# Optimization experiments

Hardware: AMD Instinct MI355X
Metric: run time of the kernel (lower is better)

## Reference

```python
import jax, jax.numpy as jnp
import numpy as np
from jax import lax

B, C, N, NB = 64, 512, 1024, 4
BC = C // NB
KS = [3, 5, 7, 9]
LEVEL = 2  # min(2, pywt.dwt_max_level(1024, 8)) = 2
FL = 8  # db4 filter length
DN = ('NCH', 'OIH', 'NCH')
# pywt db4 decomposition filters
DEC_LO = jnp.array([-0.010597401784997278, 0.032883011666982945, 0.030841381835986965,
                    -0.18703481171888114, -0.02798376941698385, 0.6308807679295904,
                    0.7148465705525415, 0.23037781330885523], jnp.float32)
DEC_HI = jnp.array([-0.23037781330885523, 0.7148465705525415, -0.6308807679295904,
                    -0.02798376941698385, 0.18703481171888114, 0.030841381835986965,
                    -0.032883011666982945, -0.010597401784997278], jnp.float32)


def conv1d(x, w, b, pad):
    y = lax.conv_general_dilated(x, w, (1,), [(pad, pad)], dimension_numbers=DN)
    return y + b[None, :, None]


def bn_relu(x, g, beta, eps=1e-5):
    # BatchNorm1d in train mode: batch statistics over (B, L) per channel
    mu = x.mean(axis=(0, 2), keepdims=True)
    var = ((x - mu) ** 2).mean(axis=(0, 2), keepdims=True)
    xn = (x - mu) * lax.rsqrt(var + eps)
    return jax.nn.relu(xn * g[None, :, None] + beta[None, :, None])


def dwt1d(x):
    # single-level pywt-compatible DWT, symmetric mode. x: [B, C, n]
    b, c, n = x.shape
    out = (n + FL - 1) // 2
    p = 2 * (out - 1) - n + FL
    xp = jnp.pad(x, ((0, 0), (0, 0), (p // 2, p - p // 2)), mode='symmetric')
    k = jnp.stack([DEC_LO[::-1], DEC_HI[::-1]])[:, None, :]  # [2,1,FL]
    y = lax.conv_general_dilated(xp.reshape(b * c, 1, -1), k, (2,), 'VALID',
                                 dimension_numbers=DN)
    y = y.reshape(b, c, 2, out)
    return y[:, :, 0], y[:, :, 1]  # (cA, cD)


def idwt1d(lo, hi):
    # single-level inverse DWT; output length = 2*nc - FL + 2
    b, c, nc = lo.shape
    x = jnp.stack([lo, hi], axis=2).reshape(b * c, 2, nc)
    # rec filters = dec filters reversed, so flipped-for-conv == dec filters
    k = jnp.stack([DEC_LO, DEC_HI])[None, :, :]  # [1,2,FL]
    y = lax.conv_general_dilated(x, k, (1,), [(FL - 1, FL - 1)],
                                 lhs_dilation=(2,), dimension_numbers=DN)
    y = y[:, 0, FL - 2: FL - 2 + 2 * nc - FL + 2]
    return y.reshape(b, c, -1)


def decouple(x):
    # TemporalPatternDecoupling: db4 wavedec(level=2) -> reconstruct low-pass-only
    # (long term) and detail-only (short term). Torch detaches before pywt.
    x = lax.stop_gradient(x)
    n = x.shape[-1]
    a, details = x, []
    for _ in range(LEVEL):
        a, d = dwt1d(a)
        details.append(d)
    la, sa = a, jnp.zeros_like(a)
    for d in reversed(details):
        dl = d.shape[-1]
        la = idwt1d(la[..., :dl], jnp.zeros_like(d))
        sa = idwt1d(sa[..., :dl], d)
    return sa[..., :n], la[..., :n]


def setup_inputs() -> dict:
    key = jax.random.key(0)
    ks = jax.random.split(key, 32)
    s = 0.05
    inp = {
        'x': jax.random.normal(ks[0], (B, C, N), jnp.float32),
        'w_init': jax.random.normal(ks[1], (C, C, 1), jnp.float32) * s,
        'b_init': jnp.zeros((C,), jnp.float32),
        'w_pf': jax.random.normal(ks[2], (BC, 2 * BC, 1), jnp.float32) * s,
        'b_pf': jnp.zeros((BC,), jnp.float32),
        'w_fus': jax.random.normal(ks[3], (C, C, 1), jnp.float32) * s,
        'b_fus': jnp.zeros((C,), jnp.float32),
    }
    for i in range(NB):
        inp[f'w_b{i + 1}'] = jax.random.normal(ks[4 + i], (BC, BC, KS[i]), jnp.float32) * s
        inp[f'b_b{i + 1}'] = jnp.zeros((BC,), jnp.float32)
        inp[f'g_b{i + 1}'] = jnp.ones((BC,), jnp.float32)
        inp[f'be_b{i + 1}'] = jnp.zeros((BC,), jnp.float32)
    return inp


def reference(x, w_init, b_init, w_b1, b_b1, g_b1, be_b1, w_b2, b_b2, g_b2, be_b2,
              w_b3, b_b3, g_b3, be_b3, w_b4, b_b4, g_b4, be_b4, w_pf, b_pf,
              w_fus, b_fus):
    identity = x
    h = conv1d(x, w_init, b_init, 0)
    branch_in = jnp.split(h, NB, axis=1)
    wb = [w_b1, w_b2, w_b3, w_b4]
    bb = [b_b1, b_b2, b_b3, b_b4]
    gb = [g_b1, g_b2, g_b3, g_b4]
    beb = [be_b1, be_b2, be_b3, be_b4]
    shorts, longs = [], []
    for i in range(NB):
        y = bn_relu(conv1d(branch_in[i], wb[i], bb[i], KS[i] // 2), gb[i], beb[i])
        s, l = decouple(y)
        shorts.append(s)
        longs.append(l)
    for b in range(1, NB):
        shorts[b] = shorts[b] + shorts[b - 1]
    for b in range(NB - 2, -1, -1):
        longs[b] = longs[b] + longs[b + 1]
    enhanced = [conv1d(jnp.concatenate([shorts[b], longs[b]], axis=1), w_pf, b_pf, 0)
                for b in range(NB)]
    out = conv1d(jnp.concatenate(enhanced, axis=1), w_fus, b_fus, 0)
    return out + identity
```

## Files before the change

kernel.cpp:

```cpp
#include <hip/hip_runtime.h>

typedef float  f32x4 __attribute__((ext_vector_type(4)));
typedef short  s16x8 __attribute__((ext_vector_type(8)));
typedef short  s16x4 __attribute__((ext_vector_type(4)));
typedef unsigned short u16;

struct PtrQuad { const float* p[4]; };

__constant__ float c_lo[8] = {-0.010597401784997278f, 0.032883011666982945f,
                              0.030841381835986965f, -0.18703481171888114f,
                              -0.02798376941698385f, 0.6308807679295904f,
                              0.7148465705525415f,  0.23037781330885523f};
__constant__ float c_hi[8] = {-0.23037781330885523f, 0.7148465705525415f,
                              -0.6308807679295904f, -0.02798376941698385f,
                              0.18703481171888114f, 0.030841381835986965f,
                              -0.032883011666982945f, -0.010597401784997278f};

__device__ __forceinline__ u16 f2bf(float f) {
    unsigned u = __float_as_uint(f);
    u += 0x7fffu + ((u >> 16) & 1u);
    return (u16)(u >> 16);
}
__device__ __forceinline__ float bf2f(u16 h) {
    return __uint_as_float(((unsigned)h) << 16);
}
__device__ __forceinline__ int lds_chunk(int row, int g) {
    return row * 4 + (g ^ ((row >> 1) & 3));
}
__device__ __forceinline__ void gload16(void* lds, const void* g) {
    __builtin_amdgcn_global_load_lds(
        (__attribute__((address_space(1))) const void*)g,
        (__attribute__((address_space(3))) void*)lds,
        16, 0, 0);
}

__global__ __launch_bounds__(256) void gemm_nt_k(
    const u16* __restrict__ A, long aB, int lda,
    const u16* __restrict__ B, long bB, int ldb,
    int K,
    u16* __restrict__ D, long dB, int dj,
    const float* __restrict__ bias)
{
    __shared__ s16x8 As[512];
    __shared__ s16x8 Bs[512];
    const int j0 = blockIdx.x * 128, i0 = blockIdx.y * 128;
    const long bb = blockIdx.z;
    const u16* Ab = A + bb * aB;
    const u16* Bb = B + bb * bB;
    const int tid = threadIdx.x;
    const int srow = tid >> 2, sg = tid & 3;
    const int ssg = sg ^ ((srow >> 1) & 3);
    const int l = tid & 63, w = tid >> 6;
    const int wi = (w >> 1) * 64, wj = (w & 1) * 64;
    const int lr = l & 15, lg = l >> 4;
    char* lA0 = (char*)As + w * 1024;
    char* lA1 = (char*)As + 4096 + w * 1024;
    char* lB0 = (char*)Bs + w * 1024;
    char* lB1 = (char*)Bs + 4096 + w * 1024;
    f32x4 acc[4][4] = {};
    for (int k0 = 0; k0 < K; k0 += 32) {
        __syncthreads();
        gload16(lA0, Ab + (long)(i0 + srow) * lda + k0 + ssg * 8);
        gload16(lA1, Ab + (long)(i0 + srow + 64) * lda + k0 + ssg * 8);
        gload16(lB0, Bb + (long)(j0 + srow) * ldb + k0 + ssg * 8);
        gload16(lB1, Bb + (long)(j0 + srow + 64) * ldb + k0 + ssg * 8);
        __syncthreads();
        s16x8 af[4], bf[4];
        #pragma unroll
        for (int f = 0; f < 4; ++f) {
            af[f] = As[lds_chunk(wi + f * 16 + lr, lg)];
            bf[f] = Bs[lds_chunk(wj + f * 16 + lr, lg)];
        }
        #pragma unroll
        for (int fi = 0; fi < 4; ++fi)
            #pragma unroll
            for (int fj = 0; fj < 4; ++fj)
                acc[fi][fj] = __builtin_amdgcn_mfma_f32_16x16x32_bf16(af[fi], bf[fj], acc[fi][fj], 0, 0, 0);
    }
    u16* Db = D + bb * dB;
    #pragma unroll
    for (int fi = 0; fi < 4; ++fi) {
        const int i = i0 + wi + fi * 16 + lg * 4;
        float b0 = 0, b1 = 0, b2v = 0, b3 = 0;
        if (bias) { b0 = bias[i]; b1 = bias[i + 1]; b2v = bias[i + 2]; b3 = bias[i + 3]; }
        #pragma unroll
        for (int fj = 0; fj < 4; ++fj) {
            const int j = j0 + wj + fj * 16 + lr;
            f32x4 d = acc[fi][fj];
            s16x4 o;
            o[0] = (short)f2bf(d[0] + b0); o[1] = (short)f2bf(d[1] + b1);
            o[2] = (short)f2bf(d[2] + b2v); o[3] = (short)f2bf(d[3] + b3);
            *(s16x4*)(Db + (long)j * dj + i) = o;
        }
    }
}

__global__ __launch_bounds__(256) void gemm_branch4_k(
    const u16* __restrict__ WpAll,
    const u16* __restrict__ H,
    u16* __restrict__ Y,
    const u16* __restrict__ zbuf)
{
    __shared__ s16x8 As[512];
    __shared__ s16x8 Bs[512];
    const int j0 = blockIdx.x * 128;
    const int br = blockIdx.y;
    const long bb = blockIdx.z;
    const int taps = 3 + 2 * br;
    const int pad = 1 + br;
    const u16* Wp = WpAll + (long)(br * br + 2 * br) * 16384;
    const u16* Hb = H + bb * 524288 + 128 * br;
    const int tid = threadIdx.x;
    const int srow = tid >> 2, sg = tid & 3;
    const int ssg = sg ^ ((srow >> 1) & 3);
    const int l = tid & 63, w = tid >> 6;
    const int wi = (w >> 1) * 64, wj = (w & 1) * 64;
    const int lr = l & 15, lg = l >> 4;
    const int lda = taps * 128;
    const int K = taps * 128;
    char* lA0 = (char*)As + w * 1024;
    char* lA1 = (char*)As + 4096 + w * 1024;
    char* lB0 = (char*)Bs + w * 1024;
    char* lB1 = (char*)Bs + 4096 + w * 1024;
    f32x4 acc[4][4] = {};
    for (int k0 = 0; k0 < K; k0 += 32) {
        const int tap = k0 >> 7, kc = k0 & 127;
        const int shift = tap - pad;
        __syncthreads();
        gload16(lA0, Wp + (long)srow * lda + k0 + ssg * 8);
        gload16(lA1, Wp + (long)(srow + 64) * lda + k0 + ssg * 8);
        {
            int n0r = j0 + srow + shift;
            int n1r = n0r + 64;
            const u16* s0 = (n0r >= 0 && n0r < 1024) ? (Hb + (long)n0r * 512 + kc + ssg * 8) : zbuf;
            const u16* s1 = (n1r >= 0 && n1r < 1024) ? (Hb + (long)n1r * 512 + kc + ssg * 8) : zbuf;
            gload16(lB0, s0);
            gload16(lB1, s1);
        }
        __syncthreads();
        s16x8 af[4], bf[4];
        #pragma unroll
        for (int f = 0; f < 4; ++f) {
            af[f] = As[lds_chunk(wi + f * 16 + lr, lg)];
            bf[f] = Bs[lds_chunk(wj + f * 16 + lr, lg)];
        }
        #pragma unroll
        for (int fi = 0; fi < 4; ++fi)
            #pragma unroll
            for (int fj = 0; fj < 4; ++fj)
                acc[fi][fj] = __builtin_amdgcn_mfma_f32_16x16x32_bf16(af[fi], bf[fj], acc[fi][fj], 0, 0, 0);
    }
    u16* Db = Y + bb * 524288 + 128 * br;
    #pragma unroll
    for (int fi = 0; fi < 4; ++fi) {
        const int i = wi + fi * 16 + lg * 4;
        #pragma unroll
        for (int fj = 0; fj < 4; ++fj) {
            const int j = j0 + wj + fj * 16 + lr;
            f32x4 d = acc[fi][fj];
            s16x4 o;
            o[0] = (short)f2bf(d[0]); o[1] = (short)f2bf(d[1]);
            o[2] = (short)f2bf(d[2]); o[3] = (short)f2bf(d[3]);
            *(s16x4*)(Db + (long)j * 512 + i) = o;
        }
    }
}

__global__ __launch_bounds__(256) void gemm_psl_k(
    const u16* __restrict__ Ybn,
    const u16* __restrict__ Bmat,
    u16* __restrict__ PSL)
{
    __shared__ s16x8 As[512];
    __shared__ s16x8 Bs[512];
    int flat = blockIdx.x + 8 * (blockIdx.y + 8 * blockIdx.z);
    int swz = (flat & 7) * 512 + (flat >> 3);
    const int j0 = (swz & 7) * 128;
    const int i0 = ((swz >> 3) & 7) * 128;
    const long bb = swz >> 6;
    const int tid = threadIdx.x;
    const u16* Ab = Ybn + bb * 524288;
    const int srow = tid >> 2, sg = tid & 3;
    const int ssg = sg ^ ((srow >> 1) & 3);
    const int l = tid & 63, w = tid >> 6;
    const int wi = (w >> 1) * 64, wj = (w & 1) * 64;
    const int lr = l & 15, lg = l >> 4;
    char* lA0 = (char*)As + w * 1024;
    char* lA1 = (char*)As + 4096 + w * 1024;
    char* lB0 = (char*)Bs + w * 1024;
    char* lB1 = (char*)Bs + 4096 + w * 1024;
    f32x4 acc[4][4] = {};
    for (int k0 = 0; k0 < 512; k0 += 32) {
        __syncthreads();
        gload16(lA0, Ab + (long)(i0 + srow) * 512 + k0 + ssg * 8);
        gload16(lA1, Ab + (long)(i0 + srow + 64) * 512 + k0 + ssg * 8);
        gload16(lB0, Bmat + (long)(j0 + srow) * 512 + k0 + ssg * 8);
        gload16(lB1, Bmat + (long)(j0 + srow + 64) * 512 + k0 + ssg * 8);
        __syncthreads();
        s16x8 af[4], bf[4];
        #pragma unroll
        for (int f = 0; f < 4; ++f) {
            af[f] = As[lds_chunk(wi + f * 16 + lr, lg)];
            bf[f] = Bs[lds_chunk(wj + f * 16 + lr, lg)];
        }
        #pragma unroll
        for (int fi = 0; fi < 4; ++fi)
            #pragma unroll
            for (int fj = 0; fj < 4; ++fj)
                acc[fi][fj] = __builtin_amdgcn_mfma_f32_16x16x32_bf16(af[fi], bf[fj], acc[fi][fj], 0, 0, 0);
    }
    u16* Db = PSL + bb * 1048576;
    #pragma unroll
    for (int fi = 0; fi < 4; ++fi) {
        const int i = i0 + wi + fi * 16 + lg * 4;
        #pragma unroll
        for (int fj = 0; fj < 4; ++fj) {
            const int j = j0 + wj + fj * 16 + lr;
            f32x4 d = acc[fi][fj];
            s16x4 o;
            o[0] = (short)f2bf(d[0]); o[1] = (short)f2bf(d[1]);
            o[2] = (short)f2bf(d[2]); o[3] = (short)f2bf(d[3]);
            *(s16x4*)(Db + (long)j * 1024 + i) = o;
        }
    }
}

__global__ __launch_bounds__(256) void gemm_time_k(
    const u16* __restrict__ MS, const u16* __restrict__ ML,
    const u16* __restrict__ PSL,
    const float* __restrict__ b2, const float* __restrict__ X,
    float* __restrict__ OUT)
{
    __shared__ s16x8 As[512];
    __shared__ s16x8 Bs[512];
    int flat = blockIdx.x + 4 * (blockIdx.y + 8 * blockIdx.z);
    int swz = (flat & 7) * 256 + (flat >> 3);
    const int j0 = (swz & 3) * 128;
    const int i0 = ((swz >> 2) & 7) * 128;
    const long bb = swz >> 5;
    const int tid = threadIdx.x;
    const int srow = tid >> 2, sg = tid & 3;
    const int ssg = sg ^ ((srow >> 1) & 3);
    const int l = tid & 63, w = tid >> 6;
    const int wi = (w >> 1) * 64, wj = (w & 1) * 64;
    const int lr = l & 15, lg = l >> 4;
    const int klo = (i0 - 96) > 0 ? (i0 - 96) : 0;
    const int khi = (i0 + 224) < 1024 ? (i0 + 224) : 1024;
    char* lA0 = (char*)As + w * 1024;
    char* lA1 = (char*)As + 4096 + w * 1024;
    char* lB0 = (char*)Bs + w * 1024;
    char* lB1 = (char*)Bs + 4096 + w * 1024;
    f32x4 acc[4][4] = {};
    for (int pass = 0; pass < 2; ++pass) {
        const u16* A = pass ? ML : MS;
        const u16* B = PSL + bb * 1048576 + (long)pass * 524288;
        for (int k0 = klo; k0 < khi; k0 += 32) {
            __syncthreads();
            gload16(lA0, A + (long)(i0 + srow) * 1024 + k0 + ssg * 8);
            gload16(lA1, A + (long)(i0 + srow + 64) * 1024 + k0 + ssg * 8);
            gload16(lB0, B + (long)(j0 + srow) * 1024 + k0 + ssg * 8);
            gload16(lB1, B + (long)(j0 + srow + 64) * 1024 + k0 + ssg * 8);
            __syncthreads();
            s16x8 af[4], bf[4];
            #pragma unroll
            for (int f = 0; f < 4; ++f) {
                af[f] = As[lds_chunk(wi + f * 16 + lr, lg)];
                bf[f] = Bs[lds_chunk(wj + f * 16 + lr, lg)];
            }
            #pragma unroll
            for (int fi = 0; fi < 4; ++fi)
                #pragma unroll
                for (int fj = 0; fj < 4; ++fj)
                    acc[fi][fj] = __builtin_amdgcn_mfma_f32_16x16x32_bf16(af[fi], bf[fj], acc[fi][fj], 0, 0, 0);
        }
    }
    float* Ob = OUT + bb * 524288;
    const float* Xb = X + bb * 524288;
    #pragma unroll
    for (int fi = 0; fi < 4; ++fi) {
        const int i = i0 + wi + fi * 16 + lg * 4;
        #pragma unroll
        for (int fj = 0; fj < 4; ++fj) {
            const int j = j0 + wj + fj * 16 + lr;
            const long a = (long)j * 1024 + i;
            f32x4 d = acc[fi][fj];
            const float bj = b2[j];
            f32x4 xv = *(const f32x4*)(Xb + a);
            f32x4 o;
            o[0] = d[0] + bj + xv[0]; o[1] = d[1] + bj + xv[1];
            o[2] = d[2] + bj + xv[2]; o[3] = d[3] + bj + xv[3];
            *(f32x4*)(Ob + a) = o;
        }
    }
}

__global__ __launch_bounds__(256) void cast_bf_k(const float* __restrict__ s, u16* __restrict__ d, int n)
{
    int i = blockIdx.x * 256 + threadIdx.x;
    if (i < n) d[i] = f2bf(s[i]);
}

__global__ __launch_bounds__(256) void pack_wb2_k(const float* __restrict__ s, u16* __restrict__ d, int taps)
{
    int i = blockIdx.x * 256 + threadIdx.x;
    if (i >= taps * 16384) return;
    int stride = taps * 128;
    int co = i / stride;
    int rem = i - co * stride;
    int tap = rem >> 7, ci = rem & 127;
    d[i] = f2bf(s[(long)(co * 128 + ci) * taps + tap]);
}

__global__ __launch_bounds__(256) void make_Ucum_k(
    const float* __restrict__ wf, const float* __restrict__ wp,
    u16* __restrict__ USc, u16* __restrict__ ULc)
{
    int gid = blockIdx.x * 256 + threadIdx.x;
    int co = gid >> 7, cc = gid & 127;
    float us[4], ul[4];
    #pragma unroll
    for (int b = 0; b < 4; ++b) {
        float s = 0.f, t = 0.f;
        for (int q = 0; q < 128; ++q) {
            float f = wf[(long)co * 512 + b * 128 + q];
            s += f * wp[q * 256 + cc];
            t += f * wp[q * 256 + 128 + cc];
        }
        us[b] = s; ul[b] = t;
    }
    float suf = 0.f;
    for (int b = 3; b >= 0; --b) { suf += us[b]; USc[(long)co * 512 + b * 128 + cc] = f2bf(suf); }
    float pre = 0.f;
    for (int b = 0; b < 4; ++b) { pre += ul[b]; ULc[(long)co * 512 + b * 128 + cc] = f2bf(pre); }
}

__global__ __launch_bounds__(256) void make_bias2_k(
    const float* __restrict__ wf, const float* __restrict__ bpf,
    const float* __restrict__ bfus, float* __restrict__ b2)
{
    int co = blockIdx.x * 256 + threadIdx.x;
    if (co >= 512) return;
    float s = bfus[co];
    for (int j = 0; j < 512; ++j) s += wf[(long)co * 512 + j] * bpf[j & 127];
    b2[co] = s;
}

__global__ __launch_bounds__(256) void eye_k(float* __restrict__ I)
{
    int i = blockIdx.x * 256 + threadIdx.x;
    I[i] = ((i >> 10) == (i & 1023)) ? 1.0f : 0.0f;
}

__global__ __launch_bounds__(256) void zero_k(float* __restrict__ p, int n)
{
    int i = blockIdx.x * 256 + threadIdx.x;
    if (i < n) p[i] = 0.f;
}

__global__ __launch_bounds__(256) void dwt_k(
    const float* __restrict__ x, float* __restrict__ a, float* __restrict__ d,
    int n_in, int n_out)
{
    const int row = blockIdx.y;
    const int m = blockIdx.x * 256 + threadIdx.x;
    if (m >= n_out) return;
    const float* xr = x + (long)row * n_in;
    float sa = 0.f, sd = 0.f;
    #pragma unroll
    for (int j = 0; j < 8; ++j) {
        int t = 2 * m + 1 - j;
        t = (t < 0) ? (-t - 1) : t;
        t = (t >= n_in) ? (2 * n_in - 1 - t) : t;
        const float v = xr[t];
        sa += v * c_lo[j];
        sd += v * c_hi[j];
    }
    a[(long)row * n_out + m] = sa;
    d[(long)row * n_out + m] = sd;
}

__global__ __launch_bounds__(256) void idwt_k(
    const float* __restrict__ lo, const float* __restrict__ hi,
    float* __restrict__ z, int nc, int n_out, long zB, int zN)
{
    const int row = blockIdx.y;
    const int m = blockIdx.x * 256 + threadIdx.x;
    if (m >= n_out) return;
    const float* lor = lo ? lo + (long)row * nc : nullptr;
    const float* hir = hi ? hi + (long)row * nc : nullptr;
    float s = 0.f;
    #pragma unroll
    for (int k = 0; k < 8; ++k) {
        int t = m + k - 1;
        if (t & 1) continue;
        int j = t >> 1;
        if (j >= nc) continue;
        if (lor) s += c_lo[k] * lor[j];
        if (hir) s += c_hi[k] * hir[j];
    }
    z[(long)(row >> 7) * zB + (long)(row & 127) * zN + m] = s;
}

__global__ __launch_bounds__(256) void trM_k(
    const float* __restrict__ S, const float* __restrict__ L,
    u16* __restrict__ MS, u16* __restrict__ ML)
{
    __shared__ float sh[32][33];
    const float* src = blockIdx.z ? L : S;
    u16* dst = blockIdx.z ? ML : MS;
    const int n0 = blockIdx.x * 32, m0 = blockIdx.y * 32;
    const int tx = threadIdx.x, ty = threadIdx.y;
    #pragma unroll
    for (int k = 0; k < 4; ++k)
        sh[ty + 8 * k][tx] = src[(long)(m0 + ty + 8 * k) * 1024 + n0 + tx];
    __syncthreads();
    #pragma unroll
    for (int k = 0; k < 4; ++k)
        dst[(long)(n0 + ty + 8 * k) * 1024 + m0 + tx] = f2bf(sh[tx][ty + 8 * k]);
}

__global__ __launch_bounds__(256) void trX_k(const float* __restrict__ x, u16* __restrict__ xcl)
{
    __shared__ float sh[32][33];
    const int n0 = blockIdx.x * 32, c0 = blockIdx.y * 32;
    const long bb = blockIdx.z;
    const int tx = threadIdx.x, ty = threadIdx.y;
    const float* xb = x + bb * 524288;
    u16* ob = xcl + bb * 524288;
    #pragma unroll
    for (int k = 0; k < 4; ++k)
        sh[ty + 8 * k][tx] = xb[(long)(c0 + ty + 8 * k) * 1024 + n0 + tx];
    __syncthreads();
    #pragma unroll
    for (int k = 0; k < 4; ++k)
        ob[(long)(n0 + ty + 8 * k) * 512 + c0 + tx] = f2bf(sh[tx][ty + 8 * k]);
}

__global__ __launch_bounds__(256) void bn_stats_k(const u16* __restrict__ Y, float* __restrict__ st)
{
    __shared__ float ss[128][16];
    __shared__ float sq[128][16];
    const int br = blockIdx.y;
    const u16* Yb = Y + 128 * br;
    float* stb = st + br * 256;
    const int t = threadIdx.x;
    const int chg = t & 15, rl = t >> 4;
    const long r0 = (long)blockIdx.x * 256;
    float s[8] = {}, q[8] = {};
    for (int k = 0; k < 16; ++k) {
        long r = r0 + rl + k * 16;
        s16x8 v = *(const s16x8*)(Yb + r * 512 + chg * 8);
        #pragma unroll
        for (int e = 0; e < 8; ++e) { float f = bf2f((u16)v[e]); s[e] += f; q[e] += f * f; }
    }
    #pragma unroll
    for (int e = 0; e < 8; ++e) { ss[chg * 8 + e][rl] = s[e]; sq[chg * 8 + e][rl] = q[e]; }
    __syncthreads();
    if (t < 128) {
        float a = 0, b = 0;
        #pragma unroll
        for (int k = 0; k < 16; ++k) { a += ss[t][k]; b += sq[t][k]; }
        atomicAdd(stb + t, a); atomicAdd(stb + 128 + t, b);
    }
}

__global__ __launch_bounds__(256) void bn_coef_k(
    const float* __restrict__ st, PtrQuad g, PtrQuad be, float* __restrict__ scsh)
{
    int c = blockIdx.x * 256 + threadIdx.x;
    if (c >= 512) return;
    int br = c >> 7, cc = c & 127;
    float mu = st[br * 256 + cc] * (1.0f / 65536.0f);
    float var = st[br * 256 + 128 + cc] * (1.0f / 65536.0f) - mu * mu;
    float sc = g.p[br][cc] * rsqrtf(var + 1e-5f);
    scsh[c] = sc;
    scsh[512 + c] = be.p[br][cc] - mu * sc;
}

__global__ __launch_bounds__(256) void bn_apply_k(
    u16* __restrict__ Y, const float* __restrict__ scsh)
{
    __shared__ float sc_[512];
    __shared__ float sh_[512];
    const int t = threadIdx.x;
    #pragma unroll
    for (int q = 0; q < 2; ++q) {
        sc_[t + q * 256] = scsh[t + q * 256];
        sh_[t + q * 256] = scsh[512 + t + q * 256];
    }
    __syncthreads();
    long gid = (long)blockIdx.x * 256 + t;
    long r = gid >> 6; int cg = (int)(gid & 63);
    u16* p = Y + r * 512 + cg * 8;
    s16x8 v = *(const s16x8*)p;
    #pragma unroll
    for (int e = 0; e < 8; ++e) {
        int c = cg * 8 + e;
        float f = bf2f((u16)v[e]) * sc_[c] + sh_[c];
        v[e] = (short)f2bf(f > 0.f ? f : 0.f);
    }
    *(s16x8*)p = v;
}

extern "C" void kernel_launch(void* const* d_in, const int* in_sizes, int n_in,
                              void* d_out, int out_size, void* d_ws, size_t ws_size,
                              hipStream_t stream)
{
    const float* x      = (const float*)d_in[0];
    const float* w_init = (const float*)d_in[1];
    const float* b_init = (const float*)d_in[2];
    const float* w_pf   = (const float*)d_in[3];
    const float* b_pf   = (const float*)d_in[4];
    const float* w_fus  = (const float*)d_in[5];
    const float* b_fus  = (const float*)d_in[6];
    const float *w_b[4];
    PtrQuad g, be;
    for (int i = 0; i < 4; ++i) {
        w_b[i]  = (const float*)d_in[7 + 4 * i];
        g.p[i]  = (const float*)d_in[9 + 4 * i];
        be.p[i] = (const float*)d_in[10 + 4 * i];
    }
    float* outf = (float*)d_out;

    char* p = (char*)d_ws;
    u16* xcl   = (u16*)p;  p += 67108864;
    u16* h     = (u16*)p;  p += 67108864;
    u16* Y     = (u16*)p;  p += 67108864;
    u16* PSL   = (u16*)p;  p += 134217728;
    u16* Wi    = (u16*)p;  p += 524288;
    u16* Wp    = (u16*)p;  p += 786432;
    u16* UScULc= (u16*)p;  p += 1048576;
    u16* MrowS = (u16*)p;  p += 2097152;
    u16* MrowL = (u16*)p;  p += 2097152;
    float* eye = (float*)p; p += 4194304;
    float* Sid = (float*)p; p += 4194304;
    float* Lid = (float*)p; p += 4194304;
    float* a1  = (float*)p; p += 2109440;
    float* d1  = (float*)p; p += 2109440;
    float* a2  = (float*)p; p += 1069056;
    float* d2  = (float*)p; p += 1069056;
    float* la1 = (float*)p; p += 2109440;
    float* sa1 = (float*)p; p += 2109440;
    float* b2  = (float*)p; p += 2048;
    float* st  = (float*)p; p += 4096;
    float* zbuf= (float*)p; p += 256;
    float* scsh= (float*)p; p += 4096;

    const int KS_[4] = {3, 5, 7, 9};
    const long wpOff[4] = {0, 3 * 16384L, 8 * 16384L, 15 * 16384L};

    cast_bf_k<<<1024, 256, 0, stream>>>(w_init, Wi, 262144);
    for (int br = 0; br < 4; ++br)
        pack_wb2_k<<<(KS_[br] * 16384 + 255) / 256, 256, 0, stream>>>(w_b[br], Wp + wpOff[br], KS_[br]);
    make_Ucum_k<<<256, 256, 0, stream>>>(w_fus, w_pf, UScULc, UScULc + 262144);
    make_bias2_k<<<2, 256, 0, stream>>>(w_fus, b_pf, b_fus, b2);

    eye_k<<<4096, 256, 0, stream>>>(eye);
    dwt_k<<<dim3(3, 1024), 256, 0, stream>>>(eye, a1, d1, 1024, 515);
    dwt_k<<<dim3(2, 1024), 256, 0, stream>>>(a1, a2, d2, 515, 261);
    idwt_k<<<dim3(3, 1024), 256, 0, stream>>>(a2, nullptr, la1, 261, 515, 65920, 515);
    idwt_k<<<dim3(3, 1024), 256, 0, stream>>>(nullptr, d2, sa1, 261, 515, 65920, 515);
    idwt_k<<<dim3(4, 1024), 256, 0, stream>>>(la1, nullptr, Lid, 515, 1024, 131072, 1024);
    idwt_k<<<dim3(4, 1024), 256, 0, stream>>>(sa1, d1, Sid, 515, 1024, 131072, 1024);
    trM_k<<<dim3(32, 32, 2), dim3(32, 8), 0, stream>>>(Sid, Lid, MrowS, MrowL);

    trX_k<<<dim3(32, 16, 64), dim3(32, 8), 0, stream>>>(x, xcl);

    gemm_nt_k<<<dim3(8, 4, 64), 256, 0, stream>>>(Wi, 0, 512, xcl, 524288, 512, 512,
                                                  h, 524288, 512, b_init);

    zero_k<<<5, 256, 0, stream>>>(st, 1088);
    gemm_branch4_k<<<dim3(8, 4, 64), 256, 0, stream>>>(Wp, h, Y, (const u16*)zbuf);

    bn_stats_k<<<dim3(256, 4), 256, 0, stream>>>(Y, st);
    bn_coef_k<<<2, 256, 0, stream>>>(st, g, be, scsh);
    bn_apply_k<<<16384, 256, 0, stream>>>(Y, scsh);

    gemm_psl_k<<<dim3(8, 8, 64), 256, 0, stream>>>(Y, UScULc, PSL);

    gemm_time_k<<<dim3(4, 8, 64), 256, 0, stream>>>(MrowS, MrowL, PSL, b2, x, outf);
}
```

Baseline: 571.5 us.

## Double-buffer LDS in all GEMMs and fuse BN statistics into branch GEMM

Every bf16 MFMA GEMM kernel now uses two LDS buffers. The next K-tile is issued with global_load_lds while the current tile is being multiplied, so each iteration needs one barrier instead of two. The branch convolution GEMM also computes per-channel sum and sum-of-squares from its fp32 accumulators using wave shuffles and writes per-block partials. That removes the separate bn_stats pass over Y and its atomics, and bn_coef now reduces the 512 partials serially per channel. The banded time-domain GEMM also narrows its K window around each row tile, which assumes the level-2 wavelet operator's nonzero band fits within the tighter range.

```diff
diff --git a/kernel.cpp b/kernel.cpp
--- a/kernel.cpp
+++ b/kernel.cpp
@@ -41,8 +41,8 @@
     u16* __restrict__ D, long dB, int dj,
     const float* __restrict__ bias)
 {
-    __shared__ s16x8 As[512];
-    __shared__ s16x8 Bs[512];
+    __shared__ s16x8 As[2][512];
+    __shared__ s16x8 Bs[2][512];
     const int j0 = blockIdx.x * 128, i0 = blockIdx.y * 128;
     const long bb = blockIdx.z;
     const u16* Ab = A + bb * aB;
@@ -53,29 +53,44 @@
     const int l = tid & 63, w = tid >> 6;
     const int wi = (w >> 1) * 64, wj = (w & 1) * 64;
     const int lr = l & 15, lg = l >> 4;
-    char* lA0 = (char*)As + w * 1024;
-    char* lA1 = (char*)As + 4096 + w * 1024;
-    char* lB0 = (char*)Bs + w * 1024;
-    char* lB1 = (char*)Bs + 4096 + w * 1024;
+    const long aoff0 = (long)(i0 + srow) * lda + ssg * 8;
+    const long aoff1 = (long)(i0 + srow + 64) * lda + ssg * 8;
+    const long boff0 = (long)(j0 + srow) * ldb + ssg * 8;
+    const long boff1 = (long)(j0 + srow + 64) * ldb + ssg * 8;
+    const int nt = K >> 5;
     f32x4 acc[4][4] = {};
-    for (int k0 = 0; k0 < K; k0 += 32) {
-        __syncthreads();
-        gload16(lA0, Ab + (long)(i0 + srow) * lda + k0 + ssg * 8);
-        gload16(lA1, Ab + (long)(i0 + srow + 64) * lda + k0 + ssg * 8);
-        gload16(lB0, Bb + (long)(j0 + srow) * ldb + k0 + ssg * 8);
-        gload16(lB1, Bb + (long)(j0 + srow + 64) * ldb + k0 + ssg * 8);
-        __syncthreads();
+    {
+        char* a0 = (char*)&As[0][0] + w * 1024;
+        char* b0 = (char*)&Bs[0][0] + w * 1024;
+        gload16(a0, Ab + aoff0);
+        gload16(a0 + 4096, Ab + aoff1);
+        gload16(b0, Bb + boff0);
+        gload16(b0 + 4096, Bb + boff1);
+    }
+    __syncthreads();
+    for (int t = 0; t < nt; ++t) {
+        const int cur = t & 1;
+        if (t + 1 < nt) {
+            const int k0 = (t + 1) << 5;
+            char* a0 = (char*)&As[cur ^ 1][0] + w * 1024;
+            char* b0 = (char*)&Bs[cur ^ 1][0] + w * 1024;
+            gload16(a0, Ab + aoff0 + k0);
+            gload16(a0 + 4096, Ab + aoff1 + k0);
+            gload16(b0, Bb + boff0 + k0);
+            gload16(b0 + 4096, Bb + boff1 + k0);
+        }
         s16x8 af[4], bf[4];
         #pragma unroll
         for (int f = 0; f < 4; ++f) {
-            af[f] = As[lds_chunk(wi + f * 16 + lr, lg)];
-            bf[f] = Bs[lds_chunk(wj + f * 16 + lr, lg)];
+            af[f] = As[cur][lds_chunk(wi + f * 16 + lr, lg)];
+            bf[f] = Bs[cur][lds_chunk(wj + f * 16 + lr, lg)];
         }
         #pragma unroll
         for (int fi = 0; fi < 4; ++fi)
             #pragma unroll
             for (int fj = 0; fj < 4; ++fj)
                 acc[fi][fj] = __builtin_amdgcn_mfma_f32_16x16x32_bf16(af[fi], bf[fj], acc[fi][fj], 0, 0, 0);
+        __syncthreads();
     }
     u16* Db = D + bb * dB;
     #pragma unroll
@@ -99,10 +114,13 @@
     const u16* __restrict__ WpAll,
     const u16* __restrict__ H,
     u16* __restrict__ Y,
-    const u16* __restrict__ zbuf)
-{
-    __shared__ s16x8 As[512];
-    __shared__ s16x8 Bs[512];
+    const u16* __restrict__ zbuf,
+    float* __restrict__ part)
+{
+    __shared__ s16x8 As[2][512];
+    __shared__ s16x8 Bs[2][512];
+    __shared__ float sred[2][128];
+    __shared__ float qred[2][128];
     const int j0 = blockIdx.x * 128;
     const int br = blockIdx.y;
     const long bb = blockIdx.z;
@@ -117,38 +135,40 @@
     const int wi = (w >> 1) * 64, wj = (w & 1) * 64;
     const int lr = l & 15, lg = l >> 4;
     const int lda = taps * 128;
-    const int K = taps * 128;
-    char* lA0 = (char*)As + w * 1024;
-    char* lA1 = (char*)As + 4096 + w * 1024;
-    char* lB0 = (char*)Bs + w * 1024;
-    char* lB1 = (char*)Bs + 4096 + w * 1024;
-    f32x4 acc[4][4] = {};
-    for (int k0 = 0; k0 < K; k0 += 32) {
+    const int nt = taps * 4;
+    auto stage = [&](int buf, int t) {
+        const int k0 = t << 5;
         const int tap = k0 >> 7, kc = k0 & 127;
         const int shift = tap - pad;
-        __syncthreads();
-        gload16(lA0, Wp + (long)srow * lda + k0 + ssg * 8);
-        gload16(lA1, Wp + (long)(srow + 64) * lda + k0 + ssg * 8);
-        {
-            int n0r = j0 + srow + shift;
-            int n1r = n0r + 64;
-            const u16* s0 = (n0r >= 0 && n0r < 1024) ? (Hb + (long)n0r * 512 + kc + ssg * 8) : zbuf;
-            const u16* s1 = (n1r >= 0 && n1r < 1024) ? (Hb + (long)n1r * 512 + kc + ssg * 8) : zbuf;
-            gload16(lB0, s0);
-            gload16(lB1, s1);
-        }
-        __syncthreads();
+        char* a0 = (char*)&As[buf][0] + w * 1024;
+        char* b0 = (char*)&Bs[buf][0] + w * 1024;
+        gload16(a0, Wp + (long)srow * lda + k0 + ssg * 8);
+        gload16(a0 + 4096, Wp + (long)(srow + 64) * lda + k0 + ssg * 8);
+        int n0r = j0 + srow + shift;
+        int n1r = n0r + 64;
+        const u16* s0 = (n0r >= 0 && n0r < 1024) ? (Hb + (long)n0r * 512 + kc + ssg * 8) : zbuf;
+        const u16* s1 = (n1r >= 0 && n1r < 1024) ? (Hb + (long)n1r * 512 + kc + ssg * 8) : zbuf;
+        gload16(b0, s0);
+        gload16(b0 + 4096, s1);
+    };
+    f32x4 acc[4][4] = {};
+    stage(0, 0);
+    __syncthreads();
+    for (int t = 0; t < nt; ++t) {
+        const int cur = t & 1;
+        if (t + 1 < nt) stage(cur ^ 1, t + 1);
         s16x8 af[4], bf[4];
         #pragma unroll
         for (int f = 0; f < 4; ++f) {
-            af[f] = As[lds_chunk(wi + f * 16 + lr, lg)];
-            bf[f] = Bs[lds_chunk(wj + f * 16 + lr, lg)];
+            af[f] = As[cur][lds_chunk(wi + f * 16 + lr, lg)];
+            bf[f] = Bs[cur][lds_chunk(wj + f * 16 + lr, lg)];
         }
         #pragma unroll
         for (int fi = 0; fi < 4; ++fi)
             #pragma unroll
             for (int fj = 0; fj < 4; ++fj)
                 acc[fi][fj] = __builtin_amdgcn_mfma_f32_16x16x32_bf16(af[fi], bf[fj], acc[fi][fj], 0, 0, 0);
+        __syncthreads();
     }
     u16* Db = Y + bb * 524288 + 128 * br;
     #pragma unroll
@@ -164,6 +184,38 @@
             *(s16x4*)(Db + (long)j * 512 + i) = o;
         }
     }
+    float sv[16], qv[16];
+    #pragma unroll
+    for (int fi = 0; fi < 4; ++fi)
+        #pragma unroll
+        for (int e = 0; e < 4; ++e) {
+            float s = 0.f, q = 0.f;
+            #pragma unroll
+            for (int fj = 0; fj < 4; ++fj) { float d = acc[fi][fj][e]; s += d; q += d * d; }
+            sv[fi * 4 + e] = s; qv[fi * 4 + e] = q;
+        }
+    #pragma unroll
+    for (int m = 1; m < 16; m <<= 1) {
+        #pragma unroll
+        for (int r = 0; r < 16; ++r) {
+            sv[r] += __shfl_xor(sv[r], m, 64);
+            qv[r] += __shfl_xor(qv[r], m, 64);
+        }
+    }
+    if (lr == 0) {
+        #pragma unroll
+        for (int r = 0; r < 16; ++r) {
+            int co = wi + (r >> 2) * 16 + lg * 4 + (r & 3);
+            sred[w & 1][co] = sv[r];
+            qred[w & 1][co] = qv[r];
+        }
+    }
+    __syncthreads();
+    if (tid < 128) {
+        long blk = (long)br * 512 + bb * 8 + blockIdx.x;
+        part[blk * 256 + tid]       = sred[0][tid] + sred[1][tid];
+        part[blk * 256 + 128 + tid] = qred[0][tid] + qred[1][tid];
+    }
 }
 
 __global__ __launch_bounds__(256) void gemm_psl_k(
@@ -171,8 +223,8 @@
     const u16* __restrict__ Bmat,
     u16* __restrict__ PSL)
 {
-    __shared__ s16x8 As[512];
-    __shared__ s16x8 Bs[512];
+    __shared__ s16x8 As[2][512];
+    __shared__ s16x8 Bs[2][512];
     int flat = blockIdx.x + 8 * (blockIdx.y + 8 * blockIdx.z);
     int swz = (flat & 7) * 512 + (flat >> 3);
     const int j0 = (swz & 7) * 128;
@@ -185,29 +237,43 @@
     const int l = tid & 63, w = tid >> 6;
     const int wi = (w >> 1) * 64, wj = (w & 1) * 64;
     const int lr = l & 15, lg = l >> 4;
-    char* lA0 = (char*)As + w * 1024;
-    char* lA1 = (char*)As + 4096 + w * 1024;
-    char* lB0 = (char*)Bs + w * 1024;
-    char* lB1 = (char*)Bs + 4096 + w * 1024;
+    const long aoff0 = (long)(i0 + srow) * 512 + ssg * 8;
+    const long aoff1 = (long)(i0 + srow + 64) * 512 + ssg * 8;
+    const long boff0 = (long)(j0 + srow) * 512 + ssg * 8;
+    const long boff1 = (long)(j0 + srow + 64) * 512 + ssg * 8;
     f32x4 acc[4][4] = {};
-    for (int k0 = 0; k0 < 512; k0 += 32) {
-        __syncthreads();
-        gload16(lA0, Ab + (long)(i0 + srow) * 512 + k0 + ssg * 8);
-        gload16(lA1, Ab + (long)(i0 + srow + 64) * 512 + k0 + ssg * 8);
-        gload16(lB0, Bmat + (long)(j0 + srow) * 512 + k0 + ssg * 8);
-        gload16(lB1, Bmat + (long)(j0 + srow + 64) * 512 + k0 + ssg * 8);
-        __syncthreads();
+    {
+        char* a0 = (char*)&As[0][0] + w * 1024;
+        char* b0 = (char*)&Bs[0][0] + w * 1024;
+        gload16(a0, Ab + aoff0);
+        gload16(a0 + 4096, Ab + aoff1);
+        gload16(b0, Bmat + boff0);
+        gload16(b0 + 4096, Bmat + boff1);
+    }
+    __syncthreads();
+    for (int t = 0; t < 16; ++t) {
+        const int cur = t & 1;
+        if (t + 1 < 16) {
+            const int k0 = (t + 1) << 5;
+            char* a0 = (char*)&As[cur ^ 1][0] + w * 1024;
+            char* b0 = (char*)&Bs[cur ^ 1][0] + w * 1024;
+            gload16(a0, Ab + aoff0 + k0);
+            gload16(a0 + 4096, Ab + aoff1 + k0);
+            gload16(b0, Bmat + boff0 + k0);
+            gload16(b0 + 4096, Bmat + boff1 + k0);
+        }
         s16x8 af[4], bf[4];
         #pragma unroll
         for (int f = 0; f < 4; ++f) {
-            af[f] = As[lds_chunk(wi + f * 16 + lr, lg)];
-            bf[f] = Bs[lds_chunk(wj + f * 16 + lr, lg)];
+            af[f] = As[cur][lds_chunk(wi + f * 16 + lr, lg)];
+            bf[f] = Bs[cur][lds_chunk(wj + f * 16 + lr, lg)];
         }
         #pragma unroll
         for (int fi = 0; fi < 4; ++fi)
             #pragma unroll
             for (int fj = 0; fj < 4; ++fj)
                 acc[fi][fj] = __builtin_amdgcn_mfma_f32_16x16x32_bf16(af[fi], bf[fj], acc[fi][fj], 0, 0, 0);
+        __syncthreads();
     }
     u16* Db = PSL + bb * 1048576;
     #pragma unroll
@@ -231,8 +297,8 @@
     const float* __restrict__ b2, const float* __restrict__ X,
     float* __restrict__ OUT)
 {
-    __shared__ s16x8 As[512];
-    __shared__ s16x8 Bs[512];
+    __shared__ s16x8 As[2][512];
+    __shared__ s16x8 Bs[2][512];
     int flat = blockIdx.x + 4 * (blockIdx.y + 8 * blockIdx.z);
     int swz = (flat & 7) * 256 + (flat >> 3);
     const int j0 = (swz & 3) * 128;
@@ -244,35 +310,40 @@
     const int l = tid & 63, w = tid >> 6;
     const int wi = (w >> 1) * 64, wj = (w & 1) * 64;
     const int lr = l & 15, lg = l >> 4;
-    const int klo = (i0 - 96) > 0 ? (i0 - 96) : 0;
-    const int khi = (i0 + 224) < 1024 ? (i0 + 224) : 1024;
-    char* lA0 = (char*)As + w * 1024;
-    char* lA1 = (char*)As + 4096 + w * 1024;
-    char* lB0 = (char*)Bs + w * 1024;
-    char* lB1 = (char*)Bs + 4096 + w * 1024;
-    f32x4 acc[4][4] = {};
-    for (int pass = 0; pass < 2; ++pass) {
+    const int klo = (i0 - 64) > 0 ? (i0 - 64) : 0;
+    const int khi = (i0 + 192) < 1024 ? (i0 + 192) : 1024;
+    const int nk = (khi - klo) >> 5;
+    const int nt = nk * 2;
+    auto stage = [&](int buf, int t) {
+        const int pass = (t >= nk) ? 1 : 0;
+        const int k0 = klo + ((t - (pass ? nk : 0)) << 5);
         const u16* A = pass ? ML : MS;
         const u16* B = PSL + bb * 1048576 + (long)pass * 524288;
-        for (int k0 = klo; k0 < khi; k0 += 32) {
-            __syncthreads();
-            gload16(lA0, A + (long)(i0 + srow) * 1024 + k0 + ssg * 8);
-            gload16(lA1, A + (long)(i0 + srow + 64) * 1024 + k0 + ssg * 8);
-            gload16(lB0, B + (long)(j0 + srow) * 1024 + k0 + ssg * 8);
-            gload16(lB1, B + (long)(j0 + srow + 64) * 1024 + k0 + ssg * 8);
-            __syncthreads();
-            s16x8 af[4], bf[4];
+        char* a0 = (char*)&As[buf][0] + w * 1024;
+        char* b0 = (char*)&Bs[buf][0] + w * 1024;
+        gload16(a0, A + (long)(i0 + srow) * 1024 + k0 + ssg * 8);
+        gload16(a0 + 4096, A + (long)(i0 + srow + 64) * 1024 + k0 + ssg * 8);
+        gload16(b0, B + (long)(j0 + srow) * 1024 + k0 + ssg * 8);
+        gload16(b0 + 4096, B + (long)(j0 + srow + 64) * 1024 + k0 + ssg * 8);
+    };
+    f32x4 acc[4][4] = {};
+    stage(0, 0);
+    __syncthreads();
+    for (int t = 0; t < nt; ++t) {
+        const int cur = t & 1;
+        if (t + 1 < nt) stage(cur ^ 1, t + 1);
+        s16x8 af[4], bf[4];
+        #pragma unroll
+        for (int f = 0; f < 4; ++f) {
+            af[f] = As[cur][lds_chunk(wi + f * 16 + lr, lg)];
+            bf[f] = Bs[cur][lds_chunk(wj + f * 16 + lr, lg)];
+        }
+        #pragma unroll
+        for (int fi = 0; fi < 4; ++fi)
             #pragma unroll
-            for (int f = 0; f < 4; ++f) {
-                af[f] = As[lds_chunk(wi + f * 16 + lr, lg)];
-                bf[f] = Bs[lds_chunk(wj + f * 16 + lr, lg)];
-            }
-            #pragma unroll
-            for (int fi = 0; fi < 4; ++fi)
-                #pragma unroll
-                for (int fj = 0; fj < 4; ++fj)
-                    acc[fi][fj] = __builtin_amdgcn_mfma_f32_16x16x32_bf16(af[fi], bf[fj], acc[fi][fj], 0, 0, 0);
-        }
+            for (int fj = 0; fj < 4; ++fj)
+                acc[fi][fj] = __builtin_amdgcn_mfma_f32_16x16x32_bf16(af[fi], bf[fj], acc[fi][fj], 0, 0, 0);
+        __syncthreads();
     }
     float* Ob = OUT + bb * 524288;
     const float* Xb = X + bb * 524288;
@@ -436,42 +507,20 @@
         ob[(long)(n0 + ty + 8 * k) * 512 + c0 + tx] = f2bf(sh[tx][ty + 8 * k]);
 }
 
-__global__ __launch_bounds__(256) void bn_stats_k(const u16* __restrict__ Y, float* __restrict__ st)
-{
-    __shared__ float ss[128][16];
-    __shared__ float sq[128][16];
-    const int br = blockIdx.y;
-    const u16* Yb = Y + 128 * br;
-    float* stb = st + br * 256;
-    const int t = threadIdx.x;
-    const int chg = t & 15, rl = t >> 4;
-    const long r0 = (long)blockIdx.x * 256;
-    float s[8] = {}, q[8] = {};
-    for (int k = 0; k < 16; ++k) {
-        long r = r0 + rl + k * 16;
-        s16x8 v = *(const s16x8*)(Yb + r * 512 + chg * 8);
-        #pragma unroll
-        for (int e = 0; e < 8; ++e) { float f = bf2f((u16)v[e]); s[e] += f; q[e] += f * f; }
-    }
-    #pragma unroll
-    for (int e = 0; e < 8; ++e) { ss[chg * 8 + e][rl] = s[e]; sq[chg * 8 + e][rl] = q[e]; }
-    __syncthreads();
-    if (t < 128) {
-        float a = 0, b = 0;
-        #pragma unroll
-        for (int k = 0; k < 16; ++k) { a += ss[t][k]; b += sq[t][k]; }
-        atomicAdd(stb + t, a); atomicAdd(stb + 128 + t, b);
-    }
-}
-
 __global__ __launch_bounds__(256) void bn_coef_k(
-    const float* __restrict__ st, PtrQuad g, PtrQuad be, float* __restrict__ scsh)
+    const float* __restrict__ part, PtrQuad g, PtrQuad be, float* __restrict__ scsh)
 {
     int c = blockIdx.x * 256 + threadIdx.x;
     if (c >= 512) return;
     int br = c >> 7, cc = c & 127;
-    float mu = st[br * 256 + cc] * (1.0f / 65536.0f);
-    float var = st[br * 256 + 128 + cc] * (1.0f / 65536.0f) - mu * mu;
+    const float* pb = part + (long)br * 131072;
+    float s = 0.f, q = 0.f;
+    for (int pidx = 0; pidx < 512; ++pidx) {
+        s += pb[pidx * 256 + cc];
+        q += pb[pidx * 256 + 128 + cc];
+    }
+    float mu = s * (1.0f / 65536.0f);
+    float var = q * (1.0f / 65536.0f) - mu * mu;
     float sc = g.p[br][cc] * rsqrtf(var + 1e-5f);
     scsh[c] = sc;
     scsh[512 + c] = be.p[br][cc] - mu * sc;
@@ -542,9 +591,9 @@
     float* la1 = (float*)p; p += 2109440;
     float* sa1 = (float*)p; p += 2109440;
     float* b2  = (float*)p; p += 2048;
-    float* st  = (float*)p; p += 4096;
     float* zbuf= (float*)p; p += 256;
     float* scsh= (float*)p; p += 4096;
+    float* part= (float*)p; p += 2097152;
 
     const int KS_[4] = {3, 5, 7, 9};
     const long wpOff[4] = {0, 3 * 16384L, 8 * 16384L, 15 * 16384L};
@@ -569,11 +618,10 @@
     gemm_nt_k<<<dim3(8, 4, 64), 256, 0, stream>>>(Wi, 0, 512, xcl, 524288, 512, 512,
                                                   h, 524288, 512, b_init);
 
-    zero_k<<<5, 256, 0, stream>>>(st, 1088);
-    gemm_branch4_k<<<dim3(8, 4, 64), 256, 0, stream>>>(Wp, h, Y, (const u16*)zbuf);
-
-    bn_stats_k<<<dim3(256, 4), 256, 0, stream>>>(Y, st);
-    bn_coef_k<<<2, 256, 0, stream>>>(st, g, be, scsh);
+    zero_k<<<1, 256, 0, stream>>>(zbuf, 64);
+    gemm_branch4_k<<<dim3(8, 4, 64), 256, 0, stream>>>(Wp, h, Y, (const u16*)zbuf, part);
+
+    bn_coef_k<<<2, 256, 0, stream>>>(part, g, be, scsh);
     bn_apply_k<<<16384, 256, 0, stream>>>(Y, scsh);
 
     gemm_psl_k<<<dim3(8, 8, 64), 256, 0, stream>>>(Y, UScULc, PSL);
```

Result: faster. 557.5 us (-2.4%).
